# Optimization experiments

Measured on AMD Instinct MI355X. Metric: run time of the kernel, lower is better.

## Reference

```python
import jax, jax.numpy as jnp
import numpy as np

H = 64    # n_hidden
N = 1535  # input nodes; total graph nodes Nn = N + 1
B = 32    # batch
BN_EPS = 1e-5


def _p(key, shape, scale=0.05):
    return (jax.random.normal(key, shape, dtype=jnp.float32) * scale)


def setup_inputs() -> dict:
    key = jax.random.key(0)
    ks = jax.random.split(key, 32)
    inp = {
        'input_xx': jax.random.normal(ks[0], (B, N, 8), dtype=jnp.float32),
        'input_yy': jax.random.normal(ks[1], (B, N), dtype=jnp.float32),
        'output_xx': jax.random.normal(ks[2], (B, 1, 8), dtype=jnp.float32),
        # fc1: Linear(9, H); fc2: Linear(H, H)
        'W1': _p(ks[3], (H, 9)), 'b1': _p(ks[4], (H,)),
        'W2': _p(ks[5], (H, H)), 'b2': _p(ks[6], (H,)),
        # enc_new_x: Linear(8, H)
        'Wenc': _p(ks[7], (H, 8)), 'benc': _p(ks[8], (H,)),
        # Q, K, V: Linear(H, H)
        'WQ': _p(ks[9], (H, H)), 'bQ': _p(ks[10], (H,)),
        'WK': _p(ks[11], (H, H)), 'bK': _p(ks[12], (H,)),
        'WV': _p(ks[13], (H, H)), 'bV': _p(ks[14], (H,)),
        # QK: Linear(2H, 1) split into the q-half and k-half of its weight row
        'wQKq': _p(ks[15], (H,)), 'wQKk': _p(ks[16], (H,)),
        'bQK': _p(ks[17], ()),
        # A2N: Linear(H, H)
        'WA': _p(ks[18], (H, H)), 'bA': _p(ks[19], (H,)),
        # BatchNorm1d affine params
        'gamma': jnp.ones((H,), jnp.float32), 'beta': jnp.zeros((H,), jnp.float32),
        # heads
        'Wmu': _p(ks[20], (1, H)), 'bmu': _p(ks[21], (1,)),
        'Wsig': _p(ks[22], (1, H)), 'bsig': _p(ks[23], (1,)),
    }
    return inp


def _forward(input_xx, input_yy, output_xx, W1, b1, W2, b2, Wenc, benc,
             WQ, bQ, WK, bK, WV, bV, wQKq, wQKk, bQK, WA, bA,
             gamma, beta, Wmu, bmu, Wsig, bsig):
    # encode input nodes: cat(x, y) -> fc1 -> relu -> fc2 -> relu
    x = jnp.concatenate([input_xx, input_yy[..., None]], axis=-1)  # [B,N,9]
    h = jax.nn.relu(x @ W1.T + b1)
    h = jax.nn.relu(h @ W2.T + b2)                                  # [B,N,H]
    out_enc = jax.nn.relu(output_xx[:, 0, :] @ Wenc.T + benc)       # [B,H]
    # nodes: [Nn, B, H]  (node axis first, matching the torch list of nodes)
    nodes = jnp.concatenate([jnp.transpose(h, (1, 0, 2)), out_enc[None]], axis=0)

    def communicate(nodes):
        q = nodes @ WQ.T + bQ  # [Nn,B,H]
        k = nodes @ WK.T + bK
        v = nodes @ WV.T + bV
        # QK(cat(q,k)) decomposes additively: score[i,b,j] = q[i,b].wq + k[j,b].wk + b
        sq = q @ wQKq          # [Nn,B]
        sk = k @ wQKk          # [Nn,B]
        scores = sq[:, :, None] + sk.T[None, :, :] + bQK  # [Nn,B,Nn]
        w_att = jax.nn.softmax(scores, axis=-1)
        aggre = jnp.einsum('ibj,jbh->ibh', w_att, v)      # [Nn,B,H]
        z = aggre @ WA.T + bA
        # BatchNorm1d in training mode, applied per node over the batch axis
        mu = jnp.mean(z, axis=1, keepdims=True)
        var = jnp.var(z, axis=1, keepdims=True)
        z = (z - mu) / jnp.sqrt(var + BN_EPS) * gamma + beta
        return jax.nn.relu(z)

    for _ in range(4):
        nodes = communicate(nodes)

    agg = jnp.max(nodes, axis=0)                # [B,H]
    mu_out = agg @ Wmu.T + bmu                  # [B,1]
    sig_out = (agg @ Wsig.T + bsig) ** 2 + 0.01 # [B,1]
    return mu_out, sig_out


def reference(input_xx, input_yy, output_xx, W1, b1, W2, b2, Wenc, benc,
              WQ, bQ, WK, bK, WV, bV, wQKq, wQKk, bQK, WA, bA,
              gamma, beta, Wmu, bmu, Wsig, bsig):
    return _forward(input_xx, input_yy, output_xx, W1, b1, W2, b2, Wenc, benc,
                    WQ, bQ, WK, bK, WV, bV, wQKq, wQKk, bQK, WA, bA,
                    gamma, beta, Wmu, bmu, Wsig, bsig)
```

## Files before the change

kernel.cpp:

```cpp
#include <hip/hip_runtime.h>
#include <math.h>

#define NIN   1535
#define NN    1536
#define BB    32
#define BN_EPS 1e-5f
#define CH    64
#define NCH   24
#define NBLK  (BB * NCH)

#define WS_M    0
#define WS_S    768
#define WS_V    1536
#define WS_WAVT 50688
#define WS_BAV  54784

__device__ __forceinline__ float rdlane(float v, int l) {
  return __int_as_float(__builtin_amdgcn_readlane(__float_as_int(v), l));
}

__global__ __launch_bounds__(256) void k_main(
    const float* __restrict__ xx, const float* __restrict__ yy,
    const float* __restrict__ oxx,
    const float* __restrict__ W1, const float* __restrict__ b1,
    const float* __restrict__ W2, const float* __restrict__ b2,
    const float* __restrict__ Wenc, const float* __restrict__ benc,
    const float* __restrict__ WK, const float* __restrict__ wQKk,
    const float* __restrict__ WV, const float* __restrict__ bV,
    const float* __restrict__ WA, const float* __restrict__ bA,
    float* __restrict__ ws) {
  __shared__ float xs[512];
  __shared__ float ys[64];
  __shared__ float us[64];
  __shared__ float cm[4], cs[4];
  __shared__ float cvec[4][64];

  const int t = threadIdx.x;
  const int blk = blockIdx.x;

  if (blk == NBLK) {
    int kg = t >> 6, h = t & 63;
    float acc[16];
    #pragma unroll
    for (int kk = 0; kk < 16; kk++) acc[kk] = 0.f;
    for (int m = 0; m < 64; m++) {
      float wa = WA[h * 64 + m];
      const float4* wv = (const float4*)(WV + m * 64 + kg * 16);
      float4 w0 = wv[0], w1 = wv[1], w2 = wv[2], w3 = wv[3];
      acc[0]  += wa * w0.x; acc[1]  += wa * w0.y; acc[2]  += wa * w0.z; acc[3]  += wa * w0.w;
      acc[4]  += wa * w1.x; acc[5]  += wa * w1.y; acc[6]  += wa * w1.z; acc[7]  += wa * w1.w;
      acc[8]  += wa * w2.x; acc[9]  += wa * w2.y; acc[10] += wa * w2.z; acc[11] += wa * w2.w;
      acc[12] += wa * w3.x; acc[13] += wa * w3.y; acc[14] += wa * w3.z; acc[15] += wa * w3.w;
    }
    #pragma unroll
    for (int kk = 0; kk < 16; kk++)
      ws[WS_WAVT + (kg * 16 + kk) * 64 + h] = acc[kk];
    if (t < 64) {
      float a = bA[t];
      #pragma unroll
      for (int k = 0; k < 64; k++) a += WA[t * 64 + k] * bV[k];
      ws[WS_BAV + t] = a;
    }
    return;
  }

  const int b = blk & 31;
  const int c = blk >> 5;
  const int pp = b * NCH + c;

  for (int e = t; e < 512; e += 256) {
    int j = e >> 3, k = e & 7;
    int r0 = c * CH + j;
    xs[e] = (r0 < NIN) ? xx[((size_t)b * NIN + r0) * 8 + k] : oxx[b * 8 + k];
  }
  if (t < 64) {
    int r0 = c * CH + t;
    ys[t] = (r0 < NIN) ? yy[b * NIN + r0] : 0.f;
    float a = 0.f;
    #pragma unroll
    for (int h0 = 0; h0 < 64; h0++) a += wQKk[h0] * WK[h0 * 64 + t];
    us[t] = a;
  }
  __syncthreads();

  const int w = t >> 6, lane = t & 63;

  float w2r[64];
  {
    const float4* wr = (const float4*)(W2 + lane * 64);
    #pragma unroll
    for (int q = 0; q < 16; q++) {
      float4 v = wr[q];
      w2r[4 * q] = v.x; w2r[4 * q + 1] = v.y;
      w2r[4 * q + 2] = v.z; w2r[4 * q + 3] = v.w;
    }
  }
  float w1r[9];
  #pragma unroll
  for (int i = 0; i < 9; i++) w1r[i] = W1[lane * 9 + i];
  const float b1v = b1[lane], b2v = b2[lane], uv = us[lane];

  float m_run = -1e30f, s_run = 0.f, acc_v = 0.f;
  for (int rr = 0; rr < 16; rr++) {
    int j = w * 16 + rr;
    int r0 = c * CH + j;
    float4 x0 = *(const float4*)(xs + j * 8);
    float4 x1 = *(const float4*)(xs + j * 8 + 4);
    float h2;
    if (r0 < NIN) {
      float a = b1v;
      a += x0.x * w1r[0] + x0.y * w1r[1] + x0.z * w1r[2] + x0.w * w1r[3];
      a += x1.x * w1r[4] + x1.y * w1r[5] + x1.z * w1r[6] + x1.w * w1r[7];
      a += ys[j] * w1r[8];
      float h1v = fmaxf(a, 0.f);
      float a0 = b2v, a1 = 0.f, a2 = 0.f, a3 = 0.f;
      #pragma unroll
      for (int k = 0; k < 64; k += 4) {
        a0 += rdlane(h1v, k)     * w2r[k];
        a1 += rdlane(h1v, k + 1) * w2r[k + 1];
        a2 += rdlane(h1v, k + 2) * w2r[k + 2];
        a3 += rdlane(h1v, k + 3) * w2r[k + 3];
      }
      h2 = fmaxf((a0 + a1) + (a2 + a3), 0.f);
    } else {
      const float4* we = (const float4*)(Wenc + lane * 8);
      float4 w0 = we[0], w1v = we[1];
      float a = benc[lane];
      a += x0.x * w0.x + x0.y * w0.y + x0.z * w0.z + x0.w * w0.w;
      a += x1.x * w1v.x + x1.y * w1v.y + x1.z * w1v.z + x1.w * w1v.w;
      h2 = fmaxf(a, 0.f);
    }
    float p = h2 * uv;
    p += __shfl_xor(p, 1);  p += __shfl_xor(p, 2);  p += __shfl_xor(p, 4);
    p += __shfl_xor(p, 8);  p += __shfl_xor(p, 16); p += __shfl_xor(p, 32);
    float mn = fmaxf(m_run, p);
    float f  = __expf(m_run - mn);
    float e  = __expf(p - mn);
    s_run = s_run * f + e;
    acc_v = acc_v * f + e * h2;
    m_run = mn;
  }

  if (lane == 0) { cm[w] = m_run; cs[w] = s_run; }
  cvec[w][lane] = acc_v;
  __syncthreads();
  if (t < 64) {
    float M = fmaxf(fmaxf(cm[0], cm[1]), fmaxf(cm[2], cm[3]));
    float f0 = __expf(cm[0] - M), f1 = __expf(cm[1] - M);
    float f2 = __expf(cm[2] - M), f3 = __expf(cm[3] - M);
    ws[WS_V + pp * 64 + t] = f0 * cvec[0][t] + f1 * cvec[1][t] +
                             f2 * cvec[2][t] + f3 * cvec[3][t];
    if (t == 0) {
      ws[WS_M + pp] = M;
      ws[WS_S + pp] = f0 * cs[0] + f1 * cs[1] + f2 * cs[2] + f3 * cs[3];
    }
  }
}

__global__ __launch_bounds__(256) void k_tail(
    const float* __restrict__ ws,
    const float* __restrict__ gamma, const float* __restrict__ beta,
    const float* __restrict__ Wmu, const float* __restrict__ bmu,
    const float* __restrict__ Wsig, const float* __restrict__ bsig,
    float* __restrict__ out) {
  __shared__ float WAVT[4096];
  __shared__ float bAVs[64];
  __shared__ float Ml[768], Sl[768], wexp[768];
  __shared__ float Mb[32], iSb[32];
  __shared__ float st[32 * 66];
  __shared__ float zs[32 * 66];
  __shared__ float scs[64], shs[64];
  const int t = threadIdx.x;

  for (int e = t; e < 4096; e += 256) WAVT[e] = ws[WS_WAVT + e];
  if (t < 64) bAVs[t] = ws[WS_BAV + t];
  for (int p = t; p < 768; p += 256) {
    Ml[p] = ws[WS_M + p];
    Sl[p] = ws[WS_S + p];
  }
  __syncthreads();

  if (t < 32) {
    float m = -1e30f;
    for (int cc = 0; cc < NCH; cc++) m = fmaxf(m, Ml[t * NCH + cc]);
    Mb[t] = m;
  }
  __syncthreads();
  for (int p = t; p < 768; p += 256) wexp[p] = __expf(Ml[p] - Mb[p / NCH]);
  __syncthreads();
  if (t < 32) {
    float s = 0.f;
    for (int cc = 0; cc < NCH; cc++) {
      int p = t * NCH + cc;
      s += Sl[p] * wexp[p];
    }
    iSb[t] = 1.0f / s;
  }
  __syncthreads();
  {
    int bb = t >> 3, hg = t & 7;
    float acc[8];
    #pragma unroll
    for (int jj = 0; jj < 8; jj++) acc[jj] = 0.f;
    for (int cc = 0; cc < NCH; cc++) {
      int p = bb * NCH + cc;
      float wgt = wexp[p];
      const float* vp = ws + WS_V + p * 64 + hg;
      #pragma unroll
      for (int jj = 0; jj < 8; jj++) acc[jj] += wgt * vp[jj * 8];
    }
    float is = iSb[bb];
    #pragma unroll
    for (int jj = 0; jj < 8; jj++) st[bb * 66 + hg + 8 * jj] = acc[jj] * is;
  }
  __syncthreads();

  for (int r = 0; r < 4; r++) {
    {
      int bb = t >> 3, hg = t & 7;
      float acc[8];
      #pragma unroll
      for (int jj = 0; jj < 8; jj++) acc[jj] = bAVs[hg + 8 * jj];
      for (int k = 0; k < 64; k++) {
        float v = st[bb * 66 + k];
        const float* wp = WAVT + k * 64 + hg;
        #pragma unroll
        for (int jj = 0; jj < 8; jj++) acc[jj] += v * wp[8 * jj];
      }
      #pragma unroll
      for (int jj = 0; jj < 8; jj++) zs[bb * 66 + hg + 8 * jj] = acc[jj];
    }
    __syncthreads();
    if (t < 64) {
      float s1 = 0.f;
      for (int bb2 = 0; bb2 < BB; bb2++) s1 += zs[bb2 * 66 + t];
      float mu = s1 * (1.0f / BB);
      float s2 = 0.f;
      for (int bb2 = 0; bb2 < BB; bb2++) {
        float d = zs[bb2 * 66 + t] - mu;
        s2 += d * d;
      }
      float inv = gamma[t] / sqrtf(s2 * (1.0f / BB) + BN_EPS);
      scs[t] = inv;
      shs[t] = beta[t] - mu * inv;
    }
    __syncthreads();
    for (int e = t; e < BB * 64; e += 256) {
      int bb2 = e >> 6, hh = e & 63;
      st[bb2 * 66 + hh] = fmaxf(zs[bb2 * 66 + hh] * scs[hh] + shs[hh], 0.f);
    }
    __syncthreads();
  }

  if (t < BB) {
    const float* nr = st + t * 66;
    float m = bmu[0], sg = bsig[0];
    #pragma unroll 8
    for (int h = 0; h < 64; h++) {
      float v = nr[h];
      m += v * Wmu[h];
      sg += v * Wsig[h];
    }
    out[t] = m;
    out[BB + t] = sg * sg + 0.01f;
  }
}

extern "C" void kernel_launch(void* const* d_in, const int* in_sizes, int n_in,
                              void* d_out, int out_size, void* d_ws, size_t ws_size,
                              hipStream_t stream) {
  const float* xx   = (const float*)d_in[0];
  const float* yy   = (const float*)d_in[1];
  const float* oxx  = (const float*)d_in[2];
  const float* W1   = (const float*)d_in[3];
  const float* b1   = (const float*)d_in[4];
  const float* W2   = (const float*)d_in[5];
  const float* b2   = (const float*)d_in[6];
  const float* Wenc = (const float*)d_in[7];
  const float* benc = (const float*)d_in[8];
  const float* WK   = (const float*)d_in[11];
  const float* WV   = (const float*)d_in[13];
  const float* bV   = (const float*)d_in[14];
  const float* wQKk = (const float*)d_in[16];
  const float* WA   = (const float*)d_in[18];
  const float* bA   = (const float*)d_in[19];
  const float* gamma= (const float*)d_in[20];
  const float* beta = (const float*)d_in[21];
  const float* Wmu  = (const float*)d_in[22];
  const float* bmu  = (const float*)d_in[23];
  const float* Wsig = (const float*)d_in[24];
  const float* bsig = (const float*)d_in[25];

  float* ws  = (float*)d_ws;
  float* out = (float*)d_out;

  k_main<<<NBLK + 1, 256, 0, stream>>>(xx, yy, oxx, W1, b1, W2, b2, Wenc, benc,
                                       WK, wQKk, WV, bV, WA, bA, ws);
  k_tail<<<1, 256, 0, stream>>>(ws, gamma, beta, Wmu, bmu, Wsig, bsig, out);
}
```

Measured before the change: 148.9 us.

## Move WA·WV fold into tail kernel, split wQKk·WK across warps, widen tail

The extra block in the main kernel that computed the folded WA·WV matrix and bias is removed. That work now runs inside the single-block tail kernel, which is widened to 512 threads and keeps the result in shared memory instead of round-tripping through the workspace. In each main block, the per-block wQKk·WK reduction is split across all four wavefronts instead of one. The aim is to shorten the serial tail and the main-kernel prologue, at the cost of adding the fold's latency to the tail's critical path.

```diff
diff --git a/kernel.cpp b/kernel.cpp
--- a/kernel.cpp
+++ b/kernel.cpp
@@ -12,8 +12,6 @@
 #define WS_M    0
 #define WS_S    768
 #define WS_V    1536
-#define WS_WAVT 50688
-#define WS_BAV  54784
 
 __device__ __forceinline__ float rdlane(float v, int l) {
   return __int_as_float(__builtin_amdgcn_readlane(__float_as_int(v), l));
@@ -26,47 +24,19 @@
     const float* __restrict__ W2, const float* __restrict__ b2,
     const float* __restrict__ Wenc, const float* __restrict__ benc,
     const float* __restrict__ WK, const float* __restrict__ wQKk,
-    const float* __restrict__ WV, const float* __restrict__ bV,
-    const float* __restrict__ WA, const float* __restrict__ bA,
     float* __restrict__ ws) {
   __shared__ float xs[512];
   __shared__ float ys[64];
-  __shared__ float us[64];
+  __shared__ float up[4][64];
   __shared__ float cm[4], cs[4];
   __shared__ float cvec[4][64];
 
   const int t = threadIdx.x;
   const int blk = blockIdx.x;
-
-  if (blk == NBLK) {
-    int kg = t >> 6, h = t & 63;
-    float acc[16];
-    #pragma unroll
-    for (int kk = 0; kk < 16; kk++) acc[kk] = 0.f;
-    for (int m = 0; m < 64; m++) {
-      float wa = WA[h * 64 + m];
-      const float4* wv = (const float4*)(WV + m * 64 + kg * 16);
-      float4 w0 = wv[0], w1 = wv[1], w2 = wv[2], w3 = wv[3];
-      acc[0]  += wa * w0.x; acc[1]  += wa * w0.y; acc[2]  += wa * w0.z; acc[3]  += wa * w0.w;
-      acc[4]  += wa * w1.x; acc[5]  += wa * w1.y; acc[6]  += wa * w1.z; acc[7]  += wa * w1.w;
-      acc[8]  += wa * w2.x; acc[9]  += wa * w2.y; acc[10] += wa * w2.z; acc[11] += wa * w2.w;
-      acc[12] += wa * w3.x; acc[13] += wa * w3.y; acc[14] += wa * w3.z; acc[15] += wa * w3.w;
-    }
-    #pragma unroll
-    for (int kk = 0; kk < 16; kk++)
-      ws[WS_WAVT + (kg * 16 + kk) * 64 + h] = acc[kk];
-    if (t < 64) {
-      float a = bA[t];
-      #pragma unroll
-      for (int k = 0; k < 64; k++) a += WA[t * 64 + k] * bV[k];
-      ws[WS_BAV + t] = a;
-    }
-    return;
-  }
-
   const int b = blk & 31;
   const int c = blk >> 5;
   const int pp = b * NCH + c;
+  const int w = t >> 6, lane = t & 63;
 
   for (int e = t; e < 512; e += 256) {
     int j = e >> 3, k = e & 7;
@@ -76,14 +46,18 @@
   if (t < 64) {
     int r0 = c * CH + t;
     ys[t] = (r0 < NIN) ? yy[b * NIN + r0] : 0.f;
-    float a = 0.f;
-    #pragma unroll
-    for (int h0 = 0; h0 < 64; h0++) a += wQKk[h0] * WK[h0 * 64 + t];
-    us[t] = a;
-  }
-  __syncthreads();
-
-  const int w = t >> 6, lane = t & 63;
+  }
+  {
+    float part = 0.f;
+    #pragma unroll
+    for (int g = 0; g < 16; g++) {
+      int h0 = w * 16 + g;
+      part += wQKk[h0] * WK[h0 * 64 + lane];
+    }
+    up[w][lane] = part;
+  }
+  __syncthreads();
+  const float uv = up[0][lane] + up[1][lane] + up[2][lane] + up[3][lane];
 
   float w2r[64];
   {
@@ -98,7 +72,7 @@
   float w1r[9];
   #pragma unroll
   for (int i = 0; i < 9; i++) w1r[i] = W1[lane * 9 + i];
-  const float b1v = b1[lane], b2v = b2[lane], uv = us[lane];
+  const float b1v = b1[lane], b2v = b2[lane];
 
   float m_run = -1e30f, s_run = 0.f, acc_v = 0.f;
   for (int rr = 0; rr < 16; rr++) {
@@ -157,8 +131,10 @@
   }
 }
 
-__global__ __launch_bounds__(256) void k_tail(
+__global__ __launch_bounds__(512) void k_tail(
     const float* __restrict__ ws,
+    const float* __restrict__ WV, const float* __restrict__ bV,
+    const float* __restrict__ WA, const float* __restrict__ bA,
     const float* __restrict__ gamma, const float* __restrict__ beta,
     const float* __restrict__ Wmu, const float* __restrict__ bmu,
     const float* __restrict__ Wsig, const float* __restrict__ bsig,
@@ -172,11 +148,32 @@
   __shared__ float scs[64], shs[64];
   const int t = threadIdx.x;
 
-  for (int e = t; e < 4096; e += 256) WAVT[e] = ws[WS_WAVT + e];
-  if (t < 64) bAVs[t] = ws[WS_BAV + t];
-  for (int p = t; p < 768; p += 256) {
+  for (int p = t; p < 768; p += 512) {
     Ml[p] = ws[WS_M + p];
     Sl[p] = ws[WS_S + p];
+  }
+  {
+    int kg = t >> 6, h = t & 63;
+    float acc[8];
+    #pragma unroll
+    for (int kk = 0; kk < 8; kk++) acc[kk] = 0.f;
+    for (int m = 0; m < 64; m++) {
+      float wa = WA[h * 64 + m];
+      const float4* wv = (const float4*)(WV + m * 64 + kg * 8);
+      float4 w0 = wv[0], w1 = wv[1];
+      acc[0] += wa * w0.x; acc[1] += wa * w0.y;
+      acc[2] += wa * w0.z; acc[3] += wa * w0.w;
+      acc[4] += wa * w1.x; acc[5] += wa * w1.y;
+      acc[6] += wa * w1.z; acc[7] += wa * w1.w;
+    }
+    #pragma unroll
+    for (int kk = 0; kk < 8; kk++) WAVT[(kg * 8 + kk) * 64 + h] = acc[kk];
+  }
+  if (t < 64) {
+    float a = bA[t];
+    #pragma unroll
+    for (int k = 0; k < 64; k++) a += WA[t * 64 + k] * bV[k];
+    bAVs[t] = a;
   }
   __syncthreads();
 
@@ -186,7 +183,7 @@
     Mb[t] = m;
   }
   __syncthreads();
-  for (int p = t; p < 768; p += 256) wexp[p] = __expf(Ml[p] - Mb[p / NCH]);
+  for (int p = t; p < 768; p += 512) wexp[p] = __expf(Ml[p] - Mb[p / NCH]);
   __syncthreads();
   if (t < 32) {
     float s = 0.f;
@@ -198,37 +195,37 @@
   }
   __syncthreads();
   {
-    int bb = t >> 3, hg = t & 7;
-    float acc[8];
-    #pragma unroll
-    for (int jj = 0; jj < 8; jj++) acc[jj] = 0.f;
+    int bb = t >> 4, hg = t & 15;
+    float acc[4];
+    #pragma unroll
+    for (int jj = 0; jj < 4; jj++) acc[jj] = 0.f;
     for (int cc = 0; cc < NCH; cc++) {
       int p = bb * NCH + cc;
       float wgt = wexp[p];
       const float* vp = ws + WS_V + p * 64 + hg;
       #pragma unroll
-      for (int jj = 0; jj < 8; jj++) acc[jj] += wgt * vp[jj * 8];
+      for (int jj = 0; jj < 4; jj++) acc[jj] += wgt * vp[jj * 16];
     }
     float is = iSb[bb];
     #pragma unroll
-    for (int jj = 0; jj < 8; jj++) st[bb * 66 + hg + 8 * jj] = acc[jj] * is;
+    for (int jj = 0; jj < 4; jj++) st[bb * 66 + hg + 16 * jj] = acc[jj] * is;
   }
   __syncthreads();
 
   for (int r = 0; r < 4; r++) {
     {
-      int bb = t >> 3, hg = t & 7;
-      float acc[8];
-      #pragma unroll
-      for (int jj = 0; jj < 8; jj++) acc[jj] = bAVs[hg + 8 * jj];
+      int bb = t >> 4, hg = t & 15;
+      float acc[4];
+      #pragma unroll
+      for (int jj = 0; jj < 4; jj++) acc[jj] = bAVs[hg + 16 * jj];
       for (int k = 0; k < 64; k++) {
         float v = st[bb * 66 + k];
         const float* wp = WAVT + k * 64 + hg;
         #pragma unroll
-        for (int jj = 0; jj < 8; jj++) acc[jj] += v * wp[8 * jj];
+        for (int jj = 0; jj < 4; jj++) acc[jj] += v * wp[16 * jj];
       }
       #pragma unroll
-      for (int jj = 0; jj < 8; jj++) zs[bb * 66 + hg + 8 * jj] = acc[jj];
+      for (int jj = 0; jj < 4; jj++) zs[bb * 66 + hg + 16 * jj] = acc[jj];
     }
     __syncthreads();
     if (t < 64) {
@@ -245,7 +242,7 @@
       shs[t] = beta[t] - mu * inv;
     }
     __syncthreads();
-    for (int e = t; e < BB * 64; e += 256) {
+    for (int e = t; e < BB * 64; e += 512) {
       int bb2 = e >> 6, hh = e & 63;
       st[bb2 * 66 + hh] = fmaxf(zs[bb2 * 66 + hh] * scs[hh] + shs[hh], 0.f);
     }
@@ -294,7 +291,8 @@
   float* ws  = (float*)d_ws;
   float* out = (float*)d_out;
 
-  k_main<<<NBLK + 1, 256, 0, stream>>>(xx, yy, oxx, W1, b1, W2, b2, Wenc, benc,
-                                       WK, wQKk, WV, bV, WA, bA, ws);
-  k_tail<<<1, 256, 0, stream>>>(ws, gamma, beta, Wmu, bmu, Wsig, bsig, out);
-}
+  k_main<<<NBLK, 256, 0, stream>>>(xx, yy, oxx, W1, b1, W2, b2, Wenc, benc,
+                                   WK, wQKk, ws);
+  k_tail<<<1, 512, 0, stream>>>(ws, WV, bV, WA, bA, gamma, beta,
+                                Wmu, bmu, Wsig, bsig, out);
+}
```

After: 150.8 us. Within noise of the previous version (+1.3%).
